# Kernel tuning notes

Measured on AMD Instinct MI355X. Metric: run time of the kernel, lower is better.

Reference implementation:

```python
import jax, jax.numpy as jnp
import numpy as np

B, S, D, H = 4, 2048, 1024, 16
PD = D // H  # projection (head) dim


def setup_inputs() -> dict:
    key = jax.random.key(0)
    ks = jax.random.split(key, 11)
    s = 1.0 / np.sqrt(D)
    return {
        "q": jax.random.normal(ks[0], (B, S, D), jnp.float32),
        "k": jax.random.normal(ks[1], (B, S, D), jnp.float32),
        "v": jax.random.normal(ks[2], (B, S, D), jnp.float32),
        "Wq": jax.random.normal(ks[3], (D, D), jnp.float32) * s,
        "bq": jnp.zeros((D,), jnp.float32),
        "Wk": jax.random.normal(ks[4], (D, D), jnp.float32) * s,
        "bk": jnp.zeros((D,), jnp.float32),
        "Wv": jax.random.normal(ks[5], (D, D), jnp.float32) * s,
        "bv": jnp.zeros((D,), jnp.float32),
        "Wo": jax.random.normal(ks[6], (D, D), jnp.float32) * s,
        "bo": jnp.zeros((D,), jnp.float32),
        "use_causal_mask": 1,
    }


def _split_heads(x):
    # [B,S,D] -> [B,H,S,PD]
    return x.reshape(B, S, H, PD).transpose(0, 2, 1, 3)


def reference(q, k, v, Wq, bq, Wk, bk, Wv, bv, Wo, bo, use_causal_mask):
    qh = _split_heads(q @ Wq + bq)
    kh = _split_heads(k @ Wk + bk)
    vh = _split_heads(v @ Wv + bv)
    # scaled dot-product attention, O(S^2) scores materialized as in original
    logits = jnp.einsum("bhsd,bhtd->bhst", qh, kh) / jnp.sqrt(jnp.float32(PD))
    if use_causal_mask:
        # Faithful to original (buggy) mask: band_part lower-tri ones, then
        # logits += log(mask*1e-6 + 1.0) -- adds ~1e-6 where allowed, 0 where masked.
        mask = jnp.tril(jnp.ones((S, S), jnp.float32))
        logits = logits + jnp.log(mask * 1e-6 + 1.0)
    attn = jax.nn.softmax(logits, axis=-1)
    out = jnp.einsum("bhst,bhtd->bhsd", attn, vh)
    concat = out.transpose(0, 2, 1, 3).reshape(B, S, D)
    return concat @ Wo + bo
```

## Files before the change

### kernel.cpp

```cpp
#include <hip/hip_runtime.h>

#define B_ 4
#define S_ 2048
#define D_ 1024
#define H_ 16
#define PD_ 64
#define M_ 8192
#define QSCALE 0.180336880145787f

typedef __attribute__((ext_vector_type(8))) short s16x8;
typedef __attribute__((ext_vector_type(4))) short s16x4;
typedef __attribute__((ext_vector_type(4))) float f32x4;

__device__ __forceinline__ short f2bf(float f) {
    unsigned int u = __float_as_uint(f);
    u = (u + 0x7FFFu + ((u >> 16) & 1u)) >> 16;
    return (short)u;
}

__device__ __forceinline__ unsigned int cvt_pk_bf16(float lo, float hi) {
    unsigned int r;
    asm("v_cvt_pk_bf16_f32 %0, %1, %2" : "=v"(r) : "v"(lo), "v"(hi));
    return r;
}

#if __has_builtin(__builtin_amdgcn_exp2f)
__device__ __forceinline__ float fast_exp2(float x) { return __builtin_amdgcn_exp2f(x); }
#else
__device__ __forceinline__ float fast_exp2(float x) {
    float r;
    asm("v_exp_f32 %0, %1" : "=v"(r) : "v"(x));
    return r;
}
#endif

#define MFMA(a, b, c) __builtin_amdgcn_mfma_f32_16x16x32_bf16(a, b, c, 0, 0, 0)

#if __has_builtin(__builtin_amdgcn_mfma_f32_16x16x16bf16_1k)
__device__ __forceinline__ f32x4 MFMA16(s16x4 a, s16x4 b, f32x4 c) {
    return __builtin_amdgcn_mfma_f32_16x16x16bf16_1k(a, b, c, 0, 0, 0);
}
#elif __has_builtin(__builtin_amdgcn_mfma_f32_16x16x16_bf16)
typedef __attribute__((ext_vector_type(4))) __bf16 bf16x4;
__device__ __forceinline__ f32x4 MFMA16(s16x4 a, s16x4 b, f32x4 c) {
    union UA { s16x4 s; bf16x4 b; };
    UA ua, ub;
    ua.s = a; ub.s = b;
    return __builtin_amdgcn_mfma_f32_16x16x16_bf16(ua.b, ub.b, c, 0, 0, 0);
}
#else
__device__ __forceinline__ f32x4 MFMA16(s16x4 a, s16x4 b, f32x4 c) {
    asm volatile("s_nop 1\n\tv_mfma_f32_16x16x16_bf16 %0, %1, %2, %0\n\ts_nop 7\n\ts_nop 7"
                 : "+v"(c) : "v"(a), "v"(b));
    return c;
}
#endif

__device__ __forceinline__ void gload16(const short* g, short* l) {
    __builtin_amdgcn_global_load_lds(
        (const __attribute__((address_space(1))) void*)g,
        (__attribute__((address_space(3))) void*)l, 16, 0, 0);
}

__global__ __launch_bounds__(256) void cvt_kernel(
    const float* __restrict__ q, const float* __restrict__ k, const float* __restrict__ v,
    short* __restrict__ oq, short* __restrict__ ok, short* __restrict__ ov) {
    const int z = blockIdx.z;
    const float* X = (z == 0) ? q : (z == 1) ? k : v;
    short* out = (z == 0) ? oq : (z == 1) ? ok : ov;
    const float s = (z == 0) ? QSCALE : 1.0f;
    size_t i0 = ((size_t)blockIdx.x * 256 + threadIdx.x) * 8;
    const size_t stride = (size_t)1024 * 256 * 8;
#pragma unroll
    for (int it = 0; it < 4; it++, i0 += stride) {
        float4 f0 = *(const float4*)&X[i0];
        float4 f1 = *(const float4*)&X[i0 + 4];
        s16x8 o = {f2bf(f0.x * s), f2bf(f0.y * s), f2bf(f0.z * s), f2bf(f0.w * s),
                   f2bf(f1.x * s), f2bf(f1.y * s), f2bf(f1.z * s), f2bf(f1.w * s)};
        *(s16x8*)&out[i0] = o;
    }
}

__global__ void wt_kernel(const float* __restrict__ Wq, const float* __restrict__ Wk,
                          const float* __restrict__ Wv, const float* __restrict__ Wo,
                          short* __restrict__ wt) {
    const float* W = (blockIdx.z == 0) ? Wq : (blockIdx.z == 1) ? Wk
                     : (blockIdx.z == 2) ? Wv : Wo;
    short* out = wt + (size_t)blockIdx.z * (D_ * D_);
    __shared__ float tile[32][33];
    const int k0 = blockIdx.x * 32, n0 = blockIdx.y * 32;
    const int tx = threadIdx.x, ty = threadIdx.y;
#pragma unroll
    for (int i = 0; i < 4; i++)
        tile[ty + 8 * i][tx] = W[(size_t)(k0 + ty + 8 * i) * D_ + n0 + tx];
    __syncthreads();
#pragma unroll
    for (int i = 0; i < 4; i++)
        out[(size_t)(n0 + ty + 8 * i) * D_ + k0 + tx] = f2bf(tile[tx][ty + 8 * i]);
}

__device__ __forceinline__ void gemm_core(const short* __restrict__ A,
                                          const short* __restrict__ Bm,
                                          int bm, int bn, short* lds,
                                          f32x4 acc[4][4]) {
    const int tid = threadIdx.x;
    const int lane = tid & 63, wid = tid >> 6;
    const int wr = (wid >> 1) * 64, wc = (wid & 1) * 64;
    const int l15 = lane & 15, l4 = lane >> 4;

    const int rr = tid >> 2;
    const int cc = tid & 3;
    const int csw = (cc ^ ((rr >> 1) & 3)) * 8;
    const short* ap = A + (size_t)(bm + rr) * D_ + csw;
    const short* bp = Bm + (size_t)(bn + rr) * D_ + csw;
    const int ldw = wid * 512;

    const int ard = (l4 ^ ((l15 >> 1) & 3)) * 8;

#define PSTAGE(bi, kkc)                                                  \
    do {                                                                 \
        short* Lp = lds + (bi) * 8192;                                   \
        gload16(ap + (kkc), Lp + ldw);                                   \
        gload16(ap + (size_t)64 * D_ + (kkc), Lp + 2048 + ldw);          \
        gload16(bp + (kkc), Lp + 4096 + ldw);                            \
        gload16(bp + (size_t)64 * D_ + (kkc), Lp + 6144 + ldw);          \
    } while (0)

    PSTAGE(0, 0);
    PSTAGE(1, 32);

    int cur = 0;
    for (int t = 0; t < 32; t++) {
        if (t + 2 < 32) {
            int nb = cur + 2;
            if (nb >= 3) nb -= 3;
            PSTAGE(nb, (t + 2) * 32);
        }
        if (t <= 29)
            asm volatile("s_waitcnt vmcnt(8)" ::: "memory");
        else if (t == 30)
            asm volatile("s_waitcnt vmcnt(4)" ::: "memory");
        else
            asm volatile("s_waitcnt vmcnt(0)" ::: "memory");
        __builtin_amdgcn_s_barrier();

        const short* La = lds + cur * 8192;
        const short* Lb = La + 4096;
        s16x8 af[4], bf[4];
#pragma unroll
        for (int i = 0; i < 4; i++)
            af[i] = *(const s16x8*)&La[(wr + i * 16 + l15) * 32 + ard];
#pragma unroll
        for (int j = 0; j < 4; j++)
            bf[j] = *(const s16x8*)&Lb[(wc + j * 16 + l15) * 32 + ard];
#pragma unroll
        for (int i = 0; i < 4; i++)
#pragma unroll
            for (int j = 0; j < 4; j++)
                acc[i][j] = MFMA(bf[j], af[i], acc[i][j]);

        __builtin_amdgcn_s_barrier();
        cur = (cur == 2) ? 0 : cur + 1;
    }
#undef PSTAGE
}

__global__ __launch_bounds__(256) void proj_kernel(
    const short* __restrict__ xq, const short* __restrict__ xk, const short* __restrict__ xv,
    const float* __restrict__ bq, const float* __restrict__ bk, const float* __restrict__ bv,
    const short* __restrict__ wtbase, short* __restrict__ outQ, short* __restrict__ outK,
    short* __restrict__ outVT) {
    const int id = blockIdx.x;
    const int xcd = id & 7, slot = id >> 3;
    const int sb = xcd + 8 * (slot >> 6);
    const int wi = slot & 63;
    const int z = sb >> 3;
    const int bn = (wi & 7) * 128;
    const int bm = (((sb & 7) << 3) + (wi >> 3)) * 128;

    const short* A = (z == 0) ? xq : (z == 1) ? xk : xv;
    const float* bias = (z == 0) ? bq : (z == 1) ? bk : bv;
    const short* Wt = wtbase + (size_t)z * (D_ * D_);
    const float bscale = (z == 0) ? QSCALE : 1.0f;

    __shared__ __align__(16) short lds[3 * 8192];

    const int tid = threadIdx.x;
    const int lane = tid & 63, wid = tid >> 6;
    const int wr = (wid >> 1) * 64, wc = (wid & 1) * 64;
    const int l15 = lane & 15, l4 = lane >> 4;

    f32x4 acc[4][4];
#pragma unroll
    for (int i = 0; i < 4; i++)
#pragma unroll
        for (int j = 0; j < 4; j++) acc[i][j] = (f32x4){0.f, 0.f, 0.f, 0.f};

    gemm_core(A, Wt, bm, bn, lds, acc);

    if (z == 2) {
        const int b = bm >> 11, sbase = bm & (S_ - 1);
        short* T = lds;
        for (int chunk = 0; chunk < 4; chunk++) {
            __syncthreads();
            if ((wc >> 6) == (chunk >> 1)) {
                const int jbase = (chunk & 1) * 2;
#pragma unroll
                for (int jj = 0; jj < 2; jj++) {
                    const int j = jbase + jj;
                    float4 b4 = *(const float4*)&bias[bn + wc + j * 16 + l4 * 4];
                    const int prow = jj * 16 + l4 * 4;
#pragma unroll
                    for (int i = 0; i < 4; i++) {
                        const int sc2 = wr + i * 16 + l15;
                        T[(prow + 0) * 132 + sc2] = f2bf(acc[i][j][0] + b4.x);
                        T[(prow + 1) * 132 + sc2] = f2bf(acc[i][j][1] + b4.y);
                        T[(prow + 2) * 132 + sc2] = f2bf(acc[i][j][2] + b4.z);
                        T[(prow + 3) * 132 + sc2] = f2bf(acc[i][j][3] + b4.w);
                    }
                }
            }
            __syncthreads();
#pragma unroll
            for (int pass = 0; pass < 2; pass++) {
                const int r = pass * 16 + (tid >> 4);
                const int sc3 = (tid & 15) * 8;
                s16x8 vv = *(const s16x8*)&T[r * 132 + sc3];
                const int grow = b * 1024 + bn + chunk * 32 + r;
                const int kvg = sc3 & 64;
                const int c8 = (sc3 >> 3) & 7;
                const int posA = ((2 * c8) & 3) * 16 + (c8 >> 1) * 4;
                const int posB = ((2 * c8 + 1) & 3) * 16 + (c8 >> 1) * 4;
                const int sx = (r & 7) << 3;
                const s16x4* hv = (const s16x4*)&vv;
                const size_t base = (size_t)grow * S_ + sbase + kvg;
                *(s16x4*)&outVT[base + (posA ^ sx)] = hv[0];
                *(s16x4*)&outVT[base + (posB ^ sx)] = hv[1];
            }
        }
    } else {
        short* out = (z == 0) ? outQ : outK;
#pragma unroll
        for (int i = 0; i < 4; i++) {
            const int m = bm + wr + i * 16 + l15;
            const int b = m >> 11, s = m & (S_ - 1);
#pragma unroll
            for (int j = 0; j < 4; j++) {
                const int n = bn + wc + j * 16 + l4 * 4;
                float4 b4 = *(const float4*)&bias[n];
                s16x4 st;
                st[0] = f2bf(acc[i][j][0] + b4.x * bscale);
                st[1] = f2bf(acc[i][j][1] + b4.y * bscale);
                st[2] = f2bf(acc[i][j][2] + b4.z * bscale);
                st[3] = f2bf(acc[i][j][3] + b4.w * bscale);
                const int h = n >> 6, pd = n & 63;
                const int pdsw = (z == 1) ? (pd ^ ((s & 7) << 3)) : pd;
                *(s16x4*)&out[(((size_t)(b * H_ + h)) * S_ + s) * PD_ + pdsw] = st;
            }
        }
    }
}

__global__ __launch_bounds__(512, 4) void attn_kernel(
    const short* __restrict__ Qh, const short* __restrict__ Kh,
    const short* __restrict__ Vtg, short* __restrict__ aout) {
    const int did = blockIdx.x + gridDim.x * blockIdx.y;
    const int bh = (did & 7) * 8 + ((did >> 3) & 7);
    const int q0 = (did >> 6) * 128;
    const short* Qp = Qh + (size_t)bh * (S_ * PD_);
    const short* Kp = Kh + (size_t)bh * (S_ * PD_);
    const short* Vp = Vtg + (size_t)bh * (PD_ * S_);

    const int tid = threadIdx.x;
    const int lane = tid & 63, w = tid >> 6;
    const int l15 = lane & 15, l4 = lane >> 4;
    const int swz = (l15 & 7) << 3;

    __shared__ __align__(16) short Ks[2][64 * 64];
    __shared__ __align__(16) short Vs[2][64 * 64];

    s16x8 qf[2];
#pragma unroll
    for (int kk = 0; kk < 2; kk++)
        qf[kk] = *(const s16x8*)&Qp[(size_t)(q0 + w * 16 + l15) * PD_ + kk * 32 + l4 * 8];

    const s16x4 ones = {(short)0x3F80, (short)0x3F80, (short)0x3F80, (short)0x3F80};

    f32x4 oacc[4];
#pragma unroll
    for (int i = 0; i < 4; i++) oacc[i] = (f32x4){0.f, 0.f, 0.f, 0.f};
    f32x4 sacc = (f32x4){0.f, 0.f, 0.f, 0.f};

    const short* kptr = Kp + (size_t)(tid >> 3) * PD_ + (tid & 7) * 8;
    const short* vptr = Vp + (size_t)(tid >> 3) * S_ + (tid & 7) * 8;
    const int ldw = w * 512;

#define AISSUE(bsel)                     \
    do {                                 \
        gload16(kptr, &Ks[bsel][ldw]);   \
        gload16(vptr, &Vs[bsel][ldw]);   \
    } while (0)

    AISSUE(0);
    kptr += 64 * PD_;
    vptr += 64;

    int cur = 0;
    for (int t = 0; t < S_; t += 64) {
        asm volatile("s_waitcnt vmcnt(0)" ::: "memory");
        __syncthreads();
        if (t + 64 < S_) {
            AISSUE(cur ^ 1);
            kptr += 64 * PD_;
            vptr += 64;
        }
        const short* Kc = Ks[cur];
        const short* Vc = Vs[cur];

        f32x4 s4[4];
#pragma unroll
        for (int n4 = 0; n4 < 4; n4++) s4[n4] = (f32x4){0.f, 0.f, 0.f, 0.f};
        __builtin_amdgcn_s_setprio(1);
#pragma unroll
        for (int n4 = 0; n4 < 4; n4++)
#pragma unroll
            for (int kk = 0; kk < 2; kk++) {
                s16x8 kf = *(const s16x8*)&Kc[(n4 * 16 + l15) * 64 + ((kk * 32 + l4 * 8) ^ swz)];
                s4[n4] = MFMA(kf, qf[kk], s4[n4]);
            }
        __builtin_amdgcn_s_setprio(0);

        s16x4 pf[4];
#pragma unroll
        for (int n4 = 0; n4 < 4; n4++) {
            float p0 = fast_exp2(s4[n4][0]);
            float p1 = fast_exp2(s4[n4][1]);
            float p2 = fast_exp2(s4[n4][2]);
            float p3 = fast_exp2(s4[n4][3]);
            uint2 pw;
            pw.x = cvt_pk_bf16(p0, p1);
            pw.y = cvt_pk_bf16(p2, p3);
            pf[n4] = *(s16x4*)&pw;
            sacc = MFMA16(ones, pf[n4], sacc);
        }

        __builtin_amdgcn_s_setprio(1);
#pragma unroll
        for (int i = 0; i < 4; i++) {
            const int vrow = (i * 16 + l15) * 64;
            s16x8 rv1 = *(const s16x8*)&Vc[vrow + (((l4 * 2) ^ (l15 & 7)) << 3)];
            s16x8 rv2 = *(const s16x8*)&Vc[vrow + (((l4 * 2 + 1) ^ (l15 & 7)) << 3)];
            const s16x4* h1 = (const s16x4*)&rv1;
            const s16x4* h2 = (const s16x4*)&rv2;
            oacc[i] = MFMA16(h1[0], pf[0], oacc[i]);
            oacc[i] = MFMA16(h1[1], pf[1], oacc[i]);
            oacc[i] = MFMA16(h2[0], pf[2], oacc[i]);
            oacc[i] = MFMA16(h2[1], pf[3], oacc[i]);
        }
        __builtin_amdgcn_s_setprio(0);
        cur ^= 1;
    }
#undef AISSUE

    const float inv = 1.0f / sacc[0];
    const int qrow = q0 + w * 16 + l15;
    const int bb = bh >> 4, hh = bh & 15;
#pragma unroll
    for (int i = 0; i < 4; i++) {
        s16x4 st;
        st[0] = f2bf(oacc[i][0] * inv);
        st[1] = f2bf(oacc[i][1] * inv);
        st[2] = f2bf(oacc[i][2] * inv);
        st[3] = f2bf(oacc[i][3] * inv);
        *(s16x4*)&aout[((size_t)(bb * S_ + qrow)) * D_ + hh * PD_ + i * 16 + l4 * 4] = st;
    }
}

__global__ __launch_bounds__(256) void out_kernel(
    const short* __restrict__ A, const short* __restrict__ Wt,
    const float* __restrict__ bo, float* __restrict__ out) {
    __shared__ __align__(16) short lds[3 * 8192];

    const int bm = blockIdx.x * 128, bn = blockIdx.y * 128;
    const int tid = threadIdx.x;
    const int lane = tid & 63, wid = tid >> 6;
    const int wr = (wid >> 1) * 64, wc = (wid & 1) * 64;
    const int l15 = lane & 15, l4 = lane >> 4;

    f32x4 acc[4][4];
#pragma unroll
    for (int i = 0; i < 4; i++)
#pragma unroll
        for (int j = 0; j < 4; j++) acc[i][j] = (f32x4){0.f, 0.f, 0.f, 0.f};

    gemm_core(A, Wt, bm, bn, lds, acc);

#pragma unroll
    for (int i = 0; i < 4; i++) {
        const int m = bm + wr + i * 16 + l15;
#pragma unroll
        for (int j = 0; j < 4; j++) {
            const int n = bn + wc + j * 16 + l4 * 4;
            float4 b4 = *(const float4*)&bo[n];
            float4 st;
            st.x = acc[i][j][0] + b4.x;
            st.y = acc[i][j][1] + b4.y;
            st.z = acc[i][j][2] + b4.z;
            st.w = acc[i][j][3] + b4.w;
            *(float4*)&out[(size_t)m * D_ + n] = st;
        }
    }
}

extern "C" void kernel_launch(void* const* d_in, const int* in_sizes, int n_in,
                              void* d_out, int out_size, void* d_ws, size_t ws_size,
                              hipStream_t stream) {
    const float* q  = (const float*)d_in[0];
    const float* k  = (const float*)d_in[1];
    const float* v  = (const float*)d_in[2];
    const float* Wq = (const float*)d_in[3];
    const float* bq = (const float*)d_in[4];
    const float* Wk = (const float*)d_in[5];
    const float* bk = (const float*)d_in[6];
    const float* Wv = (const float*)d_in[7];
    const float* bv = (const float*)d_in[8];
    const float* Wo = (const float*)d_in[9];
    const float* bo = (const float*)d_in[10];

    const size_t TEN = (size_t)M_ * D_;
    short* ws  = (short*)d_ws;
    short* wt  = ws;
    short* qh  = ws + 4 * (size_t)D_ * D_;
    short* kh  = qh + TEN;
    short* vtg = kh + TEN;
    short* xbk = vtg + TEN;
    short* xbv = xbk + TEN;
    short* xbq = (short*)d_out;
    short* ao  = xbk;
    float* out = (float*)d_out;

    hipLaunchKernelGGL(cvt_kernel, dim3(1024, 1, 3), dim3(256, 1, 1), 0, stream,
                       q, k, v, xbq, xbk, xbv);
    hipLaunchKernelGGL(wt_kernel, dim3(32, 32, 4), dim3(32, 8, 1), 0, stream,
                       Wq, Wk, Wv, Wo, wt);
    hipLaunchKernelGGL(proj_kernel, dim3(1536, 1, 1), dim3(256, 1, 1), 0, stream,
                       xbq, xbk, xbv, bq, bk, bv, wt, qh, kh, vtg);
    hipLaunchKernelGGL(attn_kernel, dim3(16, 64, 1), dim3(512, 1, 1), 0, stream,
                       qh, kh, vtg, ao);
    hipLaunchKernelGGL(out_kernel, dim3(64, 8, 1), dim3(256, 1, 1), 0, stream,
                       ao, wt + (size_t)3 * D_ * D_, bo, out);
}
```

Measured before the change: 238.0 us.

## Triple-buffer K/V tiles in attention kernel with prefetch distance two

Moves the attention kernel's K/V shared-memory staging from double to triple buffering. Loads are issued two tiles ahead, and the loop waits on vmcnt(2) instead of draining all outstanding loads each iteration. This is meant to hide global-load latency better. It costs 16KB more LDS per block, which may reduce how many blocks fit per CU under the 512x4 launch bounds.

Result: no change. 236.7 us (-0.5%).

```diff
diff --git a/kernel.cpp b/kernel.cpp
--- a/kernel.cpp
+++ b/kernel.cpp
@@ -276,8 +276,8 @@
     const int l15 = lane & 15, l4 = lane >> 4;
     const int swz = (l15 & 7) << 3;
 
-    __shared__ __align__(16) short Ks[2][64 * 64];
-    __shared__ __align__(16) short Vs[2][64 * 64];
+    __shared__ __align__(16) short Ks[3][64 * 64];
+    __shared__ __align__(16) short Vs[3][64 * 64];
 
     s16x8 qf[2];
 #pragma unroll
@@ -291,28 +291,30 @@
     for (int i = 0; i < 4; i++) oacc[i] = (f32x4){0.f, 0.f, 0.f, 0.f};
     f32x4 sacc = (f32x4){0.f, 0.f, 0.f, 0.f};
 
-    const short* kptr = Kp + (size_t)(tid >> 3) * PD_ + (tid & 7) * 8;
-    const short* vptr = Vp + (size_t)(tid >> 3) * S_ + (tid & 7) * 8;
+    const short* kbase = Kp + (size_t)(tid >> 3) * PD_ + (tid & 7) * 8;
+    const short* vbase = Vp + (size_t)(tid >> 3) * S_ + (tid & 7) * 8;
     const int ldw = w * 512;
 
-#define AISSUE(bsel)                     \
-    do {                                 \
-        gload16(kptr, &Ks[bsel][ldw]);   \
-        gload16(vptr, &Vs[bsel][ldw]);   \
+#define AISSUE(bsel, st)                                              \
+    do {                                                              \
+        gload16(kbase + (size_t)(st) * (64 * PD_), &Ks[bsel][ldw]);   \
+        gload16(vbase + (st) * 64, &Vs[bsel][ldw]);                   \
     } while (0)
 
-    AISSUE(0);
-    kptr += 64 * PD_;
-    vptr += 64;
+    AISSUE(0, 0);
+    AISSUE(1, 1);
 
     int cur = 0;
-    for (int t = 0; t < S_; t += 64) {
-        asm volatile("s_waitcnt vmcnt(0)" ::: "memory");
+    for (int t = 0; t < 32; t++) {
+        if (t < 31)
+            asm volatile("s_waitcnt vmcnt(2)" ::: "memory");
+        else
+            asm volatile("s_waitcnt vmcnt(0)" ::: "memory");
         __syncthreads();
-        if (t + 64 < S_) {
-            AISSUE(cur ^ 1);
-            kptr += 64 * PD_;
-            vptr += 64;
+        if (t + 2 < 32) {
+            int nb = cur + 2;
+            if (nb >= 3) nb -= 3;
+            AISSUE(nb, t + 2);
         }
         const short* Kc = Ks[cur];
         const short* Vc = Vs[cur];
@@ -358,7 +360,7 @@
             oacc[i] = MFMA16(h2[1], pf[3], oacc[i]);
         }
         __builtin_amdgcn_s_setprio(0);
-        cur ^= 1;
+        cur = (cur == 2) ? 0 : cur + 1;
     }
 #undef AISSUE
 
```
